# Performance work log

Measured on AMD Instinct MI355X. Metric: run time of the kernel, lower is better.

Reference implementation:

```python
import jax, jax.numpy as jnp
import numpy as np

K = 16          # top-k per pooled row
EPS = 1e-12     # tf.nn.l2_normalize epsilon


def setup_inputs() -> dict:
    key = jax.random.key(0)
    x = jax.random.normal(key, (16, 256, 128, 128), dtype=jnp.float32)
    return {"x": x}


def reference(x) -> tuple:
    # x: [B, C, H, W]; last_n_dims = 2 -> pool the trailing H*W axis.
    B, C, H, W = x.shape
    flat = x.reshape(B, C, H * W)                       # [B, C, HW]
    # tf.nn.l2_normalize(axis=-1): x / sqrt(max(sum(x^2), eps))
    sq = jnp.sum(flat * flat, axis=-1, keepdims=True)
    normed = flat * jax.lax.rsqrt(jnp.maximum(sq, EPS))  # [B, C, HW]
    top_k_value, top_k_idx = jax.lax.top_k(normed, K)    # [B, C, K]
    # decode flat indices into (h, w) coordinates (div/mod loop in original)
    h = top_k_idx // W
    w = top_k_idx % W
    coors = jnp.stack([h, w], axis=-1).astype(jnp.int32)  # [B, C, K, 2]
    return top_k_value, coors
```

## Files before the change

kernel.cpp:

```cpp
#include <hip/hip_runtime.h>


#define KSEL 16
#define HW   16384
#define QSZ  4096
#define WDIM 128
#define CAP  1024
#define CAPQ 256
#define T0   2.5f
#define NROWS 4096
#define NQ   (NROWS * 4)
#define VALS_TOTAL (NROWS * KSEL)

typedef float floatx4 __attribute__((ext_vector_type(4)));


__global__ __launch_bounds__(256) void k1_stream(const float* __restrict__ x,
                                                 float* __restrict__ qsum,
                                                 unsigned* __restrict__ qcnt,
                                                 unsigned long long* __restrict__ qcand) {
    const int b    = blockIdx.x;
    const int row  = b >> 2;
    const int q    = b & 3;
    const int t    = threadIdx.x;
    const int lane = t & 63;

    __shared__ unsigned long long s_cand[CAPQ];
    __shared__ unsigned s_cnt;
    __shared__ float s_part[4];

    if (t == 0) s_cnt = 0;
    __syncthreads();

    const floatx4* p = (const floatx4*)(x + (size_t)row * HW + q * QSZ);

    floatx4 buf[4];
    #pragma unroll
    for (int k = 0; k < 4; ++k)
        buf[k] = __builtin_nontemporal_load(&p[k * 256 + t]);

    float sumsq = 0.0f;
    #pragma unroll
    for (int k = 0; k < 4; ++k) {
        sumsq = fmaf(buf[k].x, buf[k].x, sumsq);
        sumsq = fmaf(buf[k].y, buf[k].y, sumsq);
        sumsq = fmaf(buf[k].z, buf[k].z, sumsq);
        sumsq = fmaf(buf[k].w, buf[k].w, sumsq);
    }

    unsigned msk = 0;
    #pragma unroll
    for (int k = 0; k < 4; ++k) {
        msk |= (buf[k].x > T0) ? (1u << (4 * k + 0)) : 0u;
        msk |= (buf[k].y > T0) ? (1u << (4 * k + 1)) : 0u;
        msk |= (buf[k].z > T0) ? (1u << (4 * k + 2)) : 0u;
        msk |= (buf[k].w > T0) ? (1u << (4 * k + 3)) : 0u;
    }
    unsigned base = 0;
    if (msk) base = atomicAdd(&s_cnt, (unsigned)__popc(msk));
    if (msk) {
        #pragma unroll
        for (int k = 0; k < 4; ++k) {
            #pragma unroll
            for (int c = 0; c < 4; ++c) {
                float v = (c == 0) ? buf[k].x : (c == 1) ? buf[k].y
                        : (c == 2) ? buf[k].z : buf[k].w;
                if (v > T0) {
                    if (base < CAPQ) {
                        unsigned u  = __float_as_uint(v);
                        unsigned mm = u ^ (((unsigned)((int)u >> 31)) | 0x80000000u);
                        int idx = q * QSZ + (k * 256 + t) * 4 + c;
                        s_cand[base] = ((unsigned long long)mm << 32) |
                                       (unsigned)(16383 - idx);
                    }
                    base++;
                }
            }
        }
    }

    #pragma unroll
    for (int off = 32; off > 0; off >>= 1)
        sumsq += __shfl_down(sumsq, off, 64);
    if (lane == 0) s_part[t >> 6] = sumsq;
    __syncthreads();

    unsigned cnt = s_cnt;
    unsigned wr = cnt < CAPQ ? cnt : CAPQ;
    for (unsigned i = t; i < wr; i += 256)
        qcand[(size_t)b * CAPQ + i] = s_cand[i];
    if (t == 0) {
        qcnt[b] = cnt;
        qsum[b] = s_part[0] + s_part[1] + s_part[2] + s_part[3];
    }
}

__global__ __launch_bounds__(256) void k2_select(const float* __restrict__ x,
                                                 const float* __restrict__ qsum,
                                                 const unsigned* __restrict__ qcnt,
                                                 const unsigned long long* __restrict__ qcand,
                                                 float* __restrict__ out) {
    const int row = blockIdx.x;
    const int t   = threadIdx.x;

    __shared__ unsigned long long s_cand[CAP];
    __shared__ unsigned s_qc[4];
    __shared__ float s_qs[4];
    __shared__ unsigned s_cnt;
    __shared__ float s_scale;

    if (t < 4) {
        s_qc[t] = qcnt[row * 4 + t];
        s_qs[t] = qsum[row * 4 + t];
    }
    __syncthreads();

    const unsigned c0 = s_qc[0], c1 = s_qc[1], c2 = s_qc[2], c3 = s_qc[3];
    if (t == 0)
        s_scale = 1.0f / sqrtf(fmaxf(s_qs[0] + s_qs[1] + s_qs[2] + s_qs[3], 1e-12f));
    const bool ovf = (c0 > CAPQ) | (c1 > CAPQ) | (c2 > CAPQ) | (c3 > CAPQ);
    const unsigned tot = c0 + c1 + c2 + c3;

    unsigned cnt;
    if (!ovf && tot >= KSEL && tot <= CAP) {
        const unsigned off[4] = {0u, c0, c0 + c1, c0 + c1 + c2};
        const unsigned cc[4]  = {c0, c1, c2, c3};
        #pragma unroll
        for (int q = 0; q < 4; ++q)
            for (unsigned i = t; i < cc[q]; i += 256)
                s_cand[off[q] + i] = qcand[(size_t)(row * 4 + q) * CAPQ + i];
        cnt = tot;
        __syncthreads();
    } else {
        const float* xr = x + (size_t)row * HW;
        float T = T0, lo = -3.0e38f, hi = 3.0e38f;
        cnt = 0;
        for (int it = 0; it < 32; ++it) {
            __syncthreads();
            if (t == 0) s_cnt = 0;
            __syncthreads();
            for (int i = t; i < HW; i += 256) {
                float v = xr[i];
                if (v > T) {
                    unsigned slot = atomicAdd(&s_cnt, 1u);
                    if (slot < CAP) {
                        unsigned u  = __float_as_uint(v);
                        unsigned mm = u ^ (((unsigned)((int)u >> 31)) | 0x80000000u);
                        s_cand[slot] = ((unsigned long long)mm << 32) |
                                       (unsigned)(16383 - i);
                    }
                }
            }
            __syncthreads();
            cnt = s_cnt;
            if (cnt >= KSEL && cnt <= CAP) break;
            if (cnt < KSEL) { hi = T; T = (lo < -1.0e38f) ? T - 1.0f : 0.5f * (lo + T); }
            else            { lo = T; T = (hi >  1.0e38f) ? T + 1.0f : 0.5f * (T + hi); }
        }
        if (cnt > CAP) cnt = CAP;
    }
    const float scale = s_scale;

    for (unsigned i = t; i < cnt; i += 256) {
        unsigned long long p = s_cand[i];
        unsigned m = (unsigned)(p >> 32);
        unsigned u = (m & 0x80000000u) ? (m ^ 0x80000000u) : ~m;
        float vn = __uint_as_float(u) * scale;
        unsigned u2 = __float_as_uint(vn);
        unsigned m2 = u2 ^ (((unsigned)((int)u2 >> 31)) | 0x80000000u);
        s_cand[i] = ((unsigned long long)m2 << 32) | (p & 0xFFFFFFFFull);
    }
    __syncthreads();

    for (unsigned i = t; i < cnt; i += 256) {
        unsigned long long p = s_cand[i];
        int rank = 0;
        for (unsigned j = 0; j < cnt; ++j) rank += (s_cand[j] > p) ? 1 : 0;
        if (rank < KSEL) {
            unsigned m = (unsigned)(p >> 32);
            unsigned u = (m & 0x80000000u) ? (m ^ 0x80000000u) : ~m;
            float vn = __uint_as_float(u);
            int idx = 16383 - (int)(unsigned)(p & 0xFFFFFFFFull);
            out[row * KSEL + rank] = vn;
            float* coor = out + VALS_TOTAL + ((size_t)row * KSEL + rank) * 2;
            coor[0] = (float)(idx >> 7);
            coor[1] = (float)(idx & (WDIM - 1));
        }
    }
}

extern "C" void kernel_launch(void* const* d_in, const int* in_sizes, int n_in,
                              void* d_out, int out_size, void* d_ws, size_t ws_size,
                              hipStream_t stream) {
    const float* x = (const float*)d_in[0];
    float* out = (float*)d_out;
    char* ws = (char*)d_ws;
    float* qsum = (float*)ws;
    unsigned* qcnt = (unsigned*)(ws + 64 * 1024);
    unsigned long long* qcand =
        (unsigned long long*)(ws + 128 * 1024);

    k1_stream<<<NQ, 256, 0, stream>>>(x, qsum, qcnt, qcand);
    k2_select<<<NROWS, 256, 0, stream>>>(x, qsum, qcnt, qcand, out);
}
```

Measured before the change: 337.8 us.

## Make each wavefront own a 1K-element chunk and compact candidates with wave prefix scan

The streaming kernel now gives each 64-lane wavefront its own 1024-element chunk. Candidates are compacted with a shuffle-based prefix sum and written straight to global memory, replacing the shared-memory atomic, block barriers and staging copy. Sums and counts are stored per chunk. The select kernel merges 16 chunk partials per row and drops the total-count cap check, since 16×64 equals the shared capacity. This removes block-level synchronisation and LDS traffic from the bandwidth-bound pass, at the cost of a per-chunk capacity of 64 and more small partial records.

Measured after the change: 359.5 us. 1.06x slower.

```diff
diff --git a/kernel.cpp b/kernel.cpp
--- a/kernel.cpp
+++ b/kernel.cpp
@@ -2,14 +2,15 @@
 
 
 #define KSEL 16
-#define HW   16384
-#define QSZ  4096
-#define WDIM 128
-#define CAP  1024
-#define CAPQ 256
-#define T0   2.5f
+#define HW    16384
+#define WDIM  128
+#define CHUNK 1024
+#define CAPC  64
+#define CAP   1024
+#define T0    2.5f
 #define NROWS 4096
-#define NQ   (NROWS * 4)
+#define NCHUNK (NROWS * 16)
+#define NB1   (NCHUNK / 4)
 #define VALS_TOTAL (NROWS * KSEL)
 
 typedef float floatx4 __attribute__((ext_vector_type(4)));
@@ -19,46 +20,43 @@
                                                  float* __restrict__ qsum,
                                                  unsigned* __restrict__ qcnt,
                                                  unsigned long long* __restrict__ qcand) {
-    const int b    = blockIdx.x;
-    const int row  = b >> 2;
-    const int q    = b & 3;
-    const int t    = threadIdx.x;
-    const int lane = t & 63;
+    const int t     = threadIdx.x;
+    const int lane  = t & 63;
+    const int chunk = blockIdx.x * 4 + (t >> 6);
 
-    __shared__ unsigned long long s_cand[CAPQ];
-    __shared__ unsigned s_cnt;
-    __shared__ float s_part[4];
-
-    if (t == 0) s_cnt = 0;
-    __syncthreads();
-
-    const floatx4* p = (const floatx4*)(x + (size_t)row * HW + q * QSZ);
+    const floatx4* p = (const floatx4*)(x + (size_t)chunk * CHUNK);
 
     floatx4 buf[4];
     #pragma unroll
     for (int k = 0; k < 4; ++k)
-        buf[k] = __builtin_nontemporal_load(&p[k * 256 + t]);
+        buf[k] = __builtin_nontemporal_load(&p[k * 64 + lane]);
 
     float sumsq = 0.0f;
+    unsigned msk = 0;
     #pragma unroll
     for (int k = 0; k < 4; ++k) {
         sumsq = fmaf(buf[k].x, buf[k].x, sumsq);
         sumsq = fmaf(buf[k].y, buf[k].y, sumsq);
         sumsq = fmaf(buf[k].z, buf[k].z, sumsq);
         sumsq = fmaf(buf[k].w, buf[k].w, sumsq);
-    }
-
-    unsigned msk = 0;
-    #pragma unroll
-    for (int k = 0; k < 4; ++k) {
         msk |= (buf[k].x > T0) ? (1u << (4 * k + 0)) : 0u;
         msk |= (buf[k].y > T0) ? (1u << (4 * k + 1)) : 0u;
         msk |= (buf[k].z > T0) ? (1u << (4 * k + 2)) : 0u;
         msk |= (buf[k].w > T0) ? (1u << (4 * k + 3)) : 0u;
     }
-    unsigned base = 0;
-    if (msk) base = atomicAdd(&s_cnt, (unsigned)__popc(msk));
+
+    unsigned cnum = (unsigned)__popc(msk);
+    unsigned inc = cnum;
+    #pragma unroll
+    for (int off = 1; off < 64; off <<= 1) {
+        unsigned u = (unsigned)__shfl_up((int)inc, off, 64);
+        if (lane >= off) inc += u;
+    }
+    unsigned slot = inc - cnum;
+
     if (msk) {
+        const size_t basep = (size_t)chunk * CAPC;
+        const int inrow_base = (chunk & 15) * CHUNK;
         #pragma unroll
         for (int k = 0; k < 4; ++k) {
             #pragma unroll
@@ -66,14 +64,14 @@
                 float v = (c == 0) ? buf[k].x : (c == 1) ? buf[k].y
                         : (c == 2) ? buf[k].z : buf[k].w;
                 if (v > T0) {
-                    if (base < CAPQ) {
+                    if (slot < CAPC) {
                         unsigned u  = __float_as_uint(v);
                         unsigned mm = u ^ (((unsigned)((int)u >> 31)) | 0x80000000u);
-                        int idx = q * QSZ + (k * 256 + t) * 4 + c;
-                        s_cand[base] = ((unsigned long long)mm << 32) |
-                                       (unsigned)(16383 - idx);
+                        int idx = inrow_base + (k * 64 + lane) * 4 + c;
+                        qcand[basep + slot] = ((unsigned long long)mm << 32) |
+                                              (unsigned)(16383 - idx);
                     }
-                    base++;
+                    slot++;
                 }
             }
         }
@@ -82,17 +80,8 @@
     #pragma unroll
     for (int off = 32; off > 0; off >>= 1)
         sumsq += __shfl_down(sumsq, off, 64);
-    if (lane == 0) s_part[t >> 6] = sumsq;
-    __syncthreads();
-
-    unsigned cnt = s_cnt;
-    unsigned wr = cnt < CAPQ ? cnt : CAPQ;
-    for (unsigned i = t; i < wr; i += 256)
-        qcand[(size_t)b * CAPQ + i] = s_cand[i];
-    if (t == 0) {
-        qcnt[b] = cnt;
-        qsum[b] = s_part[0] + s_part[1] + s_part[2] + s_part[3];
-    }
+    if (lane == 0)  qsum[chunk] = sumsq;
+    if (lane == 63) qcnt[chunk] = inc;
 }
 
 __global__ __launch_bounds__(256) void k2_select(const float* __restrict__ x,
@@ -104,32 +93,37 @@
     const int t   = threadIdx.x;
 
     __shared__ unsigned long long s_cand[CAP];
-    __shared__ unsigned s_qc[4];
-    __shared__ float s_qs[4];
+    __shared__ unsigned s_qc[16];
+    __shared__ float s_qs[16];
     __shared__ unsigned s_cnt;
-    __shared__ float s_scale;
 
-    if (t < 4) {
-        s_qc[t] = qcnt[row * 4 + t];
-        s_qs[t] = qsum[row * 4 + t];
+    if (t < 16) {
+        s_qc[t] = qcnt[row * 16 + t];
+        s_qs[t] = qsum[row * 16 + t];
     }
     __syncthreads();
 
-    const unsigned c0 = s_qc[0], c1 = s_qc[1], c2 = s_qc[2], c3 = s_qc[3];
-    if (t == 0)
-        s_scale = 1.0f / sqrtf(fmaxf(s_qs[0] + s_qs[1] + s_qs[2] + s_qs[3], 1e-12f));
-    const bool ovf = (c0 > CAPQ) | (c1 > CAPQ) | (c2 > CAPQ) | (c3 > CAPQ);
-    const unsigned tot = c0 + c1 + c2 + c3;
+    float tot = 0.0f;
+    unsigned cnum = 0;
+    bool ovf = false;
+    unsigned offs[16];
+    #pragma unroll
+    for (int i = 0; i < 16; ++i) {
+        offs[i] = cnum;
+        unsigned c = s_qc[i];
+        ovf |= (c > CAPC);
+        cnum += c;
+        tot += s_qs[i];
+    }
+    const float scale = 1.0f / sqrtf(fmaxf(tot, 1e-12f));
 
     unsigned cnt;
-    if (!ovf && tot >= KSEL && tot <= CAP) {
-        const unsigned off[4] = {0u, c0, c0 + c1, c0 + c1 + c2};
-        const unsigned cc[4]  = {c0, c1, c2, c3};
+    if (!ovf && cnum >= KSEL) {
         #pragma unroll
-        for (int q = 0; q < 4; ++q)
-            for (unsigned i = t; i < cc[q]; i += 256)
-                s_cand[off[q] + i] = qcand[(size_t)(row * 4 + q) * CAPQ + i];
-        cnt = tot;
+        for (int q = 0; q < 16; ++q)
+            for (unsigned i = t; i < s_qc[q]; i += 256)
+                s_cand[offs[q] + i] = qcand[(size_t)(row * 16 + q) * CAPC + i];
+        cnt = cnum;
         __syncthreads();
     } else {
         const float* xr = x + (size_t)row * HW;
@@ -159,7 +153,6 @@
         }
         if (cnt > CAP) cnt = CAP;
     }
-    const float scale = s_scale;
 
     for (unsigned i = t; i < cnt; i += 256) {
         unsigned long long p = s_cand[i];
@@ -196,10 +189,10 @@
     float* out = (float*)d_out;
     char* ws = (char*)d_ws;
     float* qsum = (float*)ws;
-    unsigned* qcnt = (unsigned*)(ws + 64 * 1024);
+    unsigned* qcnt = (unsigned*)(ws + 256 * 1024);
     unsigned long long* qcand =
-        (unsigned long long*)(ws + 128 * 1024);
+        (unsigned long long*)(ws + 512 * 1024);
 
-    k1_stream<<<NQ, 256, 0, stream>>>(x, qsum, qcnt, qcand);
+    k1_stream<<<NB1, 256, 0, stream>>>(x, qsum, qcnt, qcand);
     k2_select<<<NROWS, 256, 0, stream>>>(x, qsum, qcnt, qcand, out);
 }
```
